# Kernel optimization log

Measured on AMD Instinct MI355X. Metric: run time of the kernel, lower is better.

## Reference

```python
import jax, jax.numpy as jnp
import numpy as np

N = 20000   # nodes
E = 320000  # edges (before self loops)
H = 4       # heads
HID = 64    # hidden per head
EMB = 32    # embedding dim
IN = 4      # input features
SLOPE = 0.2   # GATv2 leaky_relu negative slope
BN_EPS = 1e-5


def _gatv2(x, Wl, bl, Wr, br, att, bias, src, dst, heads, out_ch, concat, n_nodes):
    # PyG GATv2Conv (share_weights=False, add_self_loops handled by caller)
    xl = (x @ Wl.T + bl).reshape(n_nodes, heads, out_ch)  # source transform (x_j)
    xr = (x @ Wr.T + br).reshape(n_nodes, heads, out_ch)  # target transform (x_i)
    e = jax.nn.leaky_relu(xl[src] + xr[dst], SLOPE)       # [E, H, C]
    score = jnp.einsum('ehc,hc->eh', e, att)              # [E, H]
    smax = jax.ops.segment_max(score, dst, num_segments=n_nodes)
    expw = jnp.exp(score - smax[dst])
    denom = jax.ops.segment_sum(expw, dst, num_segments=n_nodes)
    alpha = expw / (denom[dst] + 1e-16)                   # segment softmax over dst
    out = jax.ops.segment_sum(xl[src] * alpha[:, :, None], dst, num_segments=n_nodes)
    out = out.reshape(n_nodes, heads * out_ch) if concat else out.mean(axis=1)
    return out + bias


def _bn(x, gamma, beta, mean, var):
    # BatchNorm1d, eval mode (running stats)
    return gamma * (x - mean) * jax.lax.rsqrt(var + BN_EPS) + beta


def setup_inputs() -> dict:
    key = jax.random.key(0)
    ks = iter(jax.random.split(key, 40))
    d = {}
    d['x'] = jax.random.normal(next(ks), (N, IN), dtype=jnp.float32)
    d['edge_index'] = jax.random.randint(next(ks), (2, E), 0, N, dtype=jnp.int32)

    def lin(k, o, i):
        return (jax.random.normal(k, (o, i), dtype=jnp.float32) * (1.0 / np.sqrt(i)))

    d['Wl1'] = lin(next(ks), H * HID, IN); d['bl1'] = jnp.zeros((H * HID,), jnp.float32)
    d['Wr1'] = lin(next(ks), H * HID, IN); d['br1'] = jnp.zeros((H * HID,), jnp.float32)
    d['att1'] = jax.random.normal(next(ks), (H, HID), dtype=jnp.float32) * 0.1
    d['bias1'] = jnp.zeros((H * HID,), jnp.float32)
    d['bn1_g'] = jnp.ones((H * HID,), jnp.float32)
    d['bn1_b'] = jnp.zeros((H * HID,), jnp.float32)
    d['bn1_m'] = jax.random.normal(next(ks), (H * HID,), dtype=jnp.float32) * 0.1
    d['bn1_v'] = jax.random.uniform(next(ks), (H * HID,), dtype=jnp.float32) + 0.5

    d['Wl2'] = lin(next(ks), H * HID, H * HID); d['bl2'] = jnp.zeros((H * HID,), jnp.float32)
    d['Wr2'] = lin(next(ks), H * HID, H * HID); d['br2'] = jnp.zeros((H * HID,), jnp.float32)
    d['att2'] = jax.random.normal(next(ks), (H, HID), dtype=jnp.float32) * 0.1
    d['bias2'] = jnp.zeros((H * HID,), jnp.float32)
    d['bn2_g'] = jnp.ones((H * HID,), jnp.float32)
    d['bn2_b'] = jnp.zeros((H * HID,), jnp.float32)
    d['bn2_m'] = jax.random.normal(next(ks), (H * HID,), dtype=jnp.float32) * 0.1
    d['bn2_v'] = jax.random.uniform(next(ks), (H * HID,), dtype=jnp.float32) + 0.5

    # layer 3: 256 -> 32, 1 head, mean (concat=False)
    d['Wl3'] = lin(next(ks), EMB, H * HID); d['bl3'] = jnp.zeros((EMB,), jnp.float32)
    d['Wr3'] = lin(next(ks), EMB, H * HID); d['br3'] = jnp.zeros((EMB,), jnp.float32)
    d['att3'] = jax.random.normal(next(ks), (1, EMB), dtype=jnp.float32) * 0.1
    d['bias3'] = jnp.zeros((EMB,), jnp.float32)
    return d


def reference(x, edge_index,
              Wl1, bl1, Wr1, br1, att1, bias1, bn1_g, bn1_b, bn1_m, bn1_v,
              Wl2, bl2, Wr2, br2, att2, bias2, bn2_g, bn2_b, bn2_m, bn2_v,
              Wl3, bl3, Wr3, br3, att3, bias3):
    # add self loops (PyG default add_self_loops=True)
    loops = jnp.arange(N, dtype=edge_index.dtype)
    src = jnp.concatenate([edge_index[0], loops])
    dst = jnp.concatenate([edge_index[1], loops])

    h = _gatv2(x, Wl1, bl1, Wr1, br1, att1, bias1, src, dst, H, HID, True, N)
    h = jax.nn.elu(_bn(h, bn1_g, bn1_b, bn1_m, bn1_v))  # dropout: eval mode -> identity
    h = _gatv2(h, Wl2, bl2, Wr2, br2, att2, bias2, src, dst, H, HID, True, N)
    h = jax.nn.elu(_bn(h, bn2_g, bn2_b, bn2_m, bn2_v))
    z = _gatv2(h, Wl3, bl3, Wr3, br3, att3, bias3, src, dst, 1, EMB, False, N)
    return z
```

## Files before the change

kernel.cpp:

```cpp
#include <hip/hip_runtime.h>
#include <math.h>

#define NN 20000
#define EE 320000
#define ETOT (EE + NN)
#define NSCAN ((NN + 1023) / 1024)

typedef unsigned short ushort_t;
typedef unsigned int uint_t;
typedef __attribute__((ext_vector_type(8))) short bf16x8;
typedef __attribute__((ext_vector_type(4))) float f32x4;

__device__ __forceinline__ ushort_t f2bf(float f) {
  union { float f; uint_t u; } v; v.f = f;
  uint_t r = v.u + 0x7FFF + ((v.u >> 16) & 1);
  return (ushort_t)(r >> 16);
}
__device__ __forceinline__ float bf2f(uint_t hi16) {
  union { uint_t u; float f; } v; v.u = hi16 << 16;
  return v.f;
}
__device__ __forceinline__ uint_t pack2(float a, float b) {
  return (uint_t)f2bf(a) | ((uint_t)f2bf(b) << 16);
}
__device__ __forceinline__ void unpack8(uint4 u, float* x) {
  x[0] = bf2f(u.x & 0xFFFF); x[1] = bf2f(u.x >> 16);
  x[2] = bf2f(u.y & 0xFFFF); x[3] = bf2f(u.y >> 16);
  x[4] = bf2f(u.z & 0xFFFF); x[5] = bf2f(u.z >> 16);
  x[6] = bf2f(u.w & 0xFFFF); x[7] = bf2f(u.w >> 16);
}

__global__ void deg_kernel(const int* __restrict__ ei, int* __restrict__ deg) {
  int e = blockIdx.x * 256 + threadIdx.x;
  if (e >= ETOT) return;
  int dst = (e < EE) ? ei[EE + e] : (e - EE);
  atomicAdd(&deg[dst], 1);
}

__global__ __launch_bounds__(1024) void scan1_kernel(const int* __restrict__ deg,
                                                     int* __restrict__ rowptr,
                                                     int* __restrict__ partials) {
  __shared__ int wsum[16];
  const int tid = threadIdx.x;
  const int lane = tid & 63, wid = tid >> 6;
  int i = blockIdx.x * 1024 + tid;
  int v = (i < NN) ? deg[i] : 0;
  int x = v;
  #pragma unroll
  for (int off = 1; off < 64; off <<= 1) {
    int y = __shfl_up(x, off, 64);
    if (lane >= off) x += y;
  }
  if (lane == 63) wsum[wid] = x;
  __syncthreads();
  if (tid < 64) {
    int w = (tid < 16) ? wsum[tid] : 0;
    #pragma unroll
    for (int off = 1; off < 16; off <<= 1) {
      int y = __shfl_up(w, off, 64);
      if (lane >= off) w += y;
    }
    if (tid < 16) wsum[tid] = w;
  }
  __syncthreads();
  int incl = x + (wid > 0 ? wsum[wid - 1] : 0);
  if (i < NN) rowptr[i] = incl - v;
  if (tid == 1023) partials[blockIdx.x] = incl;
}

__global__ void scan2_kernel(int* __restrict__ partials, int* __restrict__ rowptr) {
  int lane = threadIdx.x;
  int v = (lane < NSCAN) ? partials[lane] : 0;
  int x = v;
  #pragma unroll
  for (int off = 1; off < 64; off <<= 1) {
    int y = __shfl_up(x, off, 64);
    if (lane >= off) x += y;
  }
  if (lane < NSCAN) partials[lane] = x - v;
  if (lane == 63) rowptr[NN] = x;
}

__global__ __launch_bounds__(1024) void scan3_kernel(int* __restrict__ rowptr,
                                                     const int* __restrict__ partials,
                                                     int* __restrict__ cursor) {
  int i = blockIdx.x * 1024 + threadIdx.x;
  if (i < NN) {
    int r = rowptr[i] + partials[blockIdx.x];
    rowptr[i] = r;
    cursor[i] = r;
  }
}

__global__ void fill_kernel(const int* __restrict__ ei, int* __restrict__ cursor,
                            int* __restrict__ csr_src) {
  int e = blockIdx.x * 256 + threadIdx.x;
  if (e >= ETOT) return;
  int src, dst;
  if (e < EE) { src = ei[e]; dst = ei[EE + e]; } else { src = dst = e - EE; }
  int slot = atomicAdd(&cursor[dst], 1);
  csr_src[slot] = src;
}

__global__ void lin1_w2bf(const float* __restrict__ x,
                          const float* __restrict__ Wl, const float* __restrict__ bl,
                          const float* __restrict__ Wr, const float* __restrict__ br,
                          ushort_t* __restrict__ xlr,
                          const float* __restrict__ W0, const float* __restrict__ W1,
                          const float* __restrict__ W2, const float* __restrict__ W3,
                          ushort_t* __restrict__ Wb) {
  if (blockIdx.x >= NN) {
    int i = (blockIdx.x - NN) * 256 + threadIdx.x;
    if (i < 65536) Wb[i] = f2bf(W0[i]);
    else if (i < 131072) Wb[i] = f2bf(W1[i - 65536]);
    else if (i < 139264) Wb[i] = f2bf(W2[i - 131072]);
    else if (i < 147456) Wb[i] = f2bf(W3[i - 139264]);
    return;
  }
  int n = blockIdx.x, o = threadIdx.x;
  float4 xv = *reinterpret_cast<const float4*>(x + (size_t)n * 4);
  float4 wl = *reinterpret_cast<const float4*>(Wl + (size_t)o * 4);
  float4 wr = *reinterpret_cast<const float4*>(Wr + (size_t)o * 4);
  xlr[(size_t)n * 512 + o]       = f2bf(wl.x * xv.x + wl.y * xv.y + wl.z * xv.z + wl.w * xv.w + bl[o]);
  xlr[(size_t)n * 512 + 256 + o] = f2bf(wr.x * xv.x + wr.y * xv.y + wr.z * xv.z + wr.w * xv.w + br[o]);
}

template<int N, int NL, int WMW, int WNW>
__global__ __launch_bounds__(WMW * WNW * 64) void gemm_mfma(
    const ushort_t* __restrict__ X, const ushort_t* __restrict__ Wb,
    const float* __restrict__ bl, const float* __restrict__ br,
    ushort_t* __restrict__ Y, int M) {
  const int wave = threadIdx.x >> 6;
  const int lane = threadIdx.x & 63;
  const int wm = wave / WNW, wn = wave % WNW;
  const int r16 = lane & 15;
  const int koff = (lane >> 4) * 8;
  const int m0 = blockIdx.x * (WMW * 64) + wm * 64;
  const int nb = blockIdx.y * (WNW * 64) + wn * 64;

  const ushort_t* xp = X + (size_t)(m0 + r16) * 256 + koff;
  const ushort_t* wp = Wb + (size_t)(nb + r16) * 256 + koff;

  f32x4 acc[4][4] = {};
  bf16x8 A[4], B[4], An[4], Bn[4];
  #pragma unroll
  for (int i = 0; i < 4; ++i) {
    A[i] = *reinterpret_cast<const bf16x8*>(xp + i * 16 * 256);
    B[i] = *reinterpret_cast<const bf16x8*>(wp + i * 16 * 256);
  }
  #pragma unroll
  for (int t = 0; t < 8; ++t) {
    if (t < 7) {
      const int k0 = (t + 1) * 32;
      #pragma unroll
      for (int i = 0; i < 4; ++i) {
        An[i] = *reinterpret_cast<const bf16x8*>(xp + i * 16 * 256 + k0);
        Bn[i] = *reinterpret_cast<const bf16x8*>(wp + i * 16 * 256 + k0);
      }
    }
    #pragma unroll
    for (int j = 0; j < 4; ++j)
      #pragma unroll
      for (int i = 0; i < 4; ++i)
        acc[j][i] = __builtin_amdgcn_mfma_f32_16x16x32_bf16(B[j], A[i], acc[j][i], 0, 0, 0);
    #pragma unroll
    for (int i = 0; i < 4; ++i) { A[i] = An[i]; B[i] = Bn[i]; }
  }

  const int nlocal = (lane >> 4) * 2;
  #pragma unroll
  for (int j = 0; j < 4; ++j) {
    const int ncol0 = nb + j * 16 + (lane >> 4) * 4;
    const float4 bv = *reinterpret_cast<const float4*>(
        (ncol0 < NL) ? (bl + ncol0) : (br + (ncol0 - NL)));
    #pragma unroll
    for (int i = 0; i < 4; ++i) {
      int m = m0 + i * 16 + r16;
      if (m < M) {
        uint2 o;
        o.x = pack2(acc[j][i][0] + bv.x, acc[j][i][1] + bv.y);
        o.y = pack2(acc[j][i][2] + bv.z, acc[j][i][3] + bv.w);
        *reinterpret_cast<uint2*>(Y + (size_t)m * N + ncol0) = o;
      }
    }
  }
}

template<bool BN_ELU>
__global__ __launch_bounds__(256) void fused_agg4(
    const ushort_t* __restrict__ xlr,
    const int* __restrict__ rowptr, const int* __restrict__ csr_src,
    const float* __restrict__ att, const float* __restrict__ bias,
    const float* __restrict__ bn_g, const float* __restrict__ bn_b,
    const float* __restrict__ bn_m, const float* __restrict__ bn_v,
    ushort_t* __restrict__ out) {
  int n = blockIdx.x * 4 + (threadIdx.x >> 6);
  if (n >= NN) return;
  int lane = threadIdx.x & 63;
  int half = lane >> 5;
  int l32 = lane & 31;

  float xr[8], at[8];
  {
    uint4 xru = reinterpret_cast<const uint4*>(xlr + (size_t)n * 512 + 256)[l32];
    unpack8(xru, xr);
    float4 a0 = reinterpret_cast<const float4*>(att)[l32 * 2];
    float4 a1 = reinterpret_cast<const float4*>(att)[l32 * 2 + 1];
    at[0] = a0.x; at[1] = a0.y; at[2] = a0.z; at[3] = a0.w;
    at[4] = a1.x; at[5] = a1.y; at[6] = a1.z; at[7] = a1.w;
  }
  int beg = rowptr[n], end = rowptr[n + 1];

  float m = -3.4e38f, d = 0.f;
  float acc[8] = {0.f, 0.f, 0.f, 0.f, 0.f, 0.f, 0.f, 0.f};

  for (int s = beg + half; s < end; s += 2) {
    int src = csr_src[s];
    uint4 xu = reinterpret_cast<const uint4*>(xlr + (size_t)src * 512)[l32];
    float x[8];
    unpack8(xu, x);
    float sc = 0.f;
    #pragma unroll
    for (int c = 0; c < 8; ++c) {
      float e = x[c] + xr[c];
      e = fmaxf(e, 0.2f * e);
      sc = fmaf(at[c], e, sc);
    }
    #pragma unroll
    for (int off = 4; off; off >>= 1) sc += __shfl_xor(sc, off, 64);
    if (__any(sc > m + 8.f)) {
      float mn = fmaxf(m, sc);
      float scl = __expf(m - mn);
      float w = __expf(sc - mn);
      #pragma unroll
      for (int c = 0; c < 8; ++c) acc[c] = fmaf(w, x[c], acc[c] * scl);
      d = d * scl + w;
      m = mn;
    } else {
      float w = __expf(sc - m);
      #pragma unroll
      for (int c = 0; c < 8; ++c) acc[c] = fmaf(w, x[c], acc[c]);
      d += w;
    }
  }

  {
    float mo = __shfl_xor(m, 32, 64);
    float doo = __shfl_xor(d, 32, 64);
    float ao[8];
    #pragma unroll
    for (int c = 0; c < 8; ++c) ao[c] = __shfl_xor(acc[c], 32, 64);
    if (doo > 0.f) {
      if (d > 0.f) {
        float mn = fmaxf(m, mo);
        float se = __expf(m - mn), so = __expf(mo - mn);
        #pragma unroll
        for (int c = 0; c < 8; ++c) acc[c] = acc[c] * se + ao[c] * so;
        d = d * se + doo * so;
      } else {
        #pragma unroll
        for (int c = 0; c < 8; ++c) acc[c] = ao[c];
        d = doo;
      }
    }
  }

  if (half == 0) {
    float inv = 1.f / (d + 1e-16f);
    float4 b0 = reinterpret_cast<const float4*>(bias)[l32 * 2];
    float4 b1 = reinterpret_cast<const float4*>(bias)[l32 * 2 + 1];
    float v[8];
    v[0] = acc[0] * inv + b0.x; v[1] = acc[1] * inv + b0.y;
    v[2] = acc[2] * inv + b0.z; v[3] = acc[3] * inv + b0.w;
    v[4] = acc[4] * inv + b1.x; v[5] = acc[5] * inv + b1.y;
    v[6] = acc[6] * inv + b1.z; v[7] = acc[7] * inv + b1.w;
    if (BN_ELU) {
      float4 g0 = reinterpret_cast<const float4*>(bn_g)[l32 * 2];
      float4 g1 = reinterpret_cast<const float4*>(bn_g)[l32 * 2 + 1];
      float4 bb0 = reinterpret_cast<const float4*>(bn_b)[l32 * 2];
      float4 bb1 = reinterpret_cast<const float4*>(bn_b)[l32 * 2 + 1];
      float4 mu0 = reinterpret_cast<const float4*>(bn_m)[l32 * 2];
      float4 mu1 = reinterpret_cast<const float4*>(bn_m)[l32 * 2 + 1];
      float4 va0 = reinterpret_cast<const float4*>(bn_v)[l32 * 2];
      float4 va1 = reinterpret_cast<const float4*>(bn_v)[l32 * 2 + 1];
      float g[8] = {g0.x, g0.y, g0.z, g0.w, g1.x, g1.y, g1.z, g1.w};
      float bb[8] = {bb0.x, bb0.y, bb0.z, bb0.w, bb1.x, bb1.y, bb1.z, bb1.w};
      float mu[8] = {mu0.x, mu0.y, mu0.z, mu0.w, mu1.x, mu1.y, mu1.z, mu1.w};
      float va[8] = {va0.x, va0.y, va0.z, va0.w, va1.x, va1.y, va1.z, va1.w};
      #pragma unroll
      for (int c = 0; c < 8; ++c) {
        float sc = g[c] * rsqrtf(va[c] + 1e-5f);
        float t = sc * (v[c] - mu[c]) + bb[c];
        v[c] = (t > 0.f) ? t : expm1f(t);
      }
    }
    uint4 o;
    o.x = pack2(v[0], v[1]);
    o.y = pack2(v[2], v[3]);
    o.z = pack2(v[4], v[5]);
    o.w = pack2(v[6], v[7]);
    reinterpret_cast<uint4*>(out + (size_t)n * 256)[l32] = o;
  }
}

__global__ __launch_bounds__(256) void fused_agg3(
    const ushort_t* __restrict__ xlr,
    const int* __restrict__ rowptr, const int* __restrict__ csr_src,
    const float* __restrict__ att, const float* __restrict__ bias,
    float* __restrict__ out) {
  int n = blockIdx.x * 4 + (threadIdx.x >> 6);
  if (n >= NN) return;
  int lane = threadIdx.x & 63;
  int grp = lane >> 4;
  int cl = lane & 15;
  uint_t xru = reinterpret_cast<const uint_t*>(xlr + (size_t)n * 64 + 32)[cl];
  float xr0 = bf2f(xru & 0xFFFF), xr1 = bf2f(xru >> 16);
  float2 atv = reinterpret_cast<const float2*>(att)[cl];
  int beg = rowptr[n], end = rowptr[n + 1];
  float m = -3.4e38f, d = 0.f, a0 = 0.f, a1 = 0.f;
  for (int s = beg + grp; s < end; s += 4) {
    int src = csr_src[s];
    uint_t xu = reinterpret_cast<const uint_t*>(xlr + (size_t)src * 64)[cl];
    float x0 = bf2f(xu & 0xFFFF), x1 = bf2f(xu >> 16);
    float e0 = x0 + xr0; e0 = fmaxf(e0, 0.2f * e0);
    float e1 = x1 + xr1; e1 = fmaxf(e1, 0.2f * e1);
    float sc = fmaf(atv.x, e0, atv.y * e1);
    #pragma unroll
    for (int off = 8; off; off >>= 1) sc += __shfl_xor(sc, off, 64);
    if (__any(sc > m + 8.f)) {
      float mn = fmaxf(m, sc);
      float scale = __expf(m - mn);
      float w = __expf(sc - mn);
      a0 = fmaf(w, x0, a0 * scale);
      a1 = fmaf(w, x1, a1 * scale);
      d = d * scale + w;
      m = mn;
    } else {
      float w = __expf(sc - m);
      a0 = fmaf(w, x0, a0);
      a1 = fmaf(w, x1, a1);
      d += w;
    }
  }
  #pragma unroll
  for (int off = 16; off <= 32; off <<= 1) {
    float mo = __shfl_xor(m, off, 64);
    float doo = __shfl_xor(d, off, 64);
    float c0 = __shfl_xor(a0, off, 64);
    float c1 = __shfl_xor(a1, off, 64);
    if (doo > 0.f) {
      if (d > 0.f) {
        float mn = fmaxf(m, mo);
        float se = __expf(m - mn), so = __expf(mo - mn);
        a0 = a0 * se + c0 * so;
        a1 = a1 * se + c1 * so;
        d = d * se + doo * so;
        m = mn;
      } else {
        a0 = c0; a1 = c1; d = doo; m = mo;
      }
    }
  }
  if (grp == 0) {
    float inv = 1.f / (d + 1e-16f);
    float2 bsv = reinterpret_cast<const float2*>(bias)[cl];
    reinterpret_cast<float2*>(out + (size_t)n * 32)[cl] =
        make_float2(a0 * inv + bsv.x, a1 * inv + bsv.y);
  }
}

extern "C" void kernel_launch(void* const* d_in, const int* in_sizes, int n_in,
                              void* d_out, int out_size, void* d_ws, size_t ws_size,
                              hipStream_t stream) {
  (void)in_sizes; (void)n_in; (void)out_size; (void)ws_size;
  const float* x  = (const float*)d_in[0];
  const int*   ei = (const int*)d_in[1];
  const float *Wl1 = (const float*)d_in[2],  *bl1 = (const float*)d_in[3],
              *Wr1 = (const float*)d_in[4],  *br1 = (const float*)d_in[5],
              *att1 = (const float*)d_in[6], *bias1 = (const float*)d_in[7],
              *g1 = (const float*)d_in[8],   *be1 = (const float*)d_in[9],
              *m1 = (const float*)d_in[10],  *v1 = (const float*)d_in[11];
  const float *Wl2 = (const float*)d_in[12], *bl2 = (const float*)d_in[13],
              *Wr2 = (const float*)d_in[14], *br2 = (const float*)d_in[15],
              *att2 = (const float*)d_in[16], *bias2 = (const float*)d_in[17],
              *g2 = (const float*)d_in[18],  *be2 = (const float*)d_in[19],
              *m2 = (const float*)d_in[20],  *v2 = (const float*)d_in[21];
  const float *Wl3 = (const float*)d_in[22], *bl3 = (const float*)d_in[23],
              *Wr3 = (const float*)d_in[24], *br3 = (const float*)d_in[25],
              *att3 = (const float*)d_in[26], *bias3 = (const float*)d_in[27];
  float* out = (float*)d_out;

  char* p = (char*)d_ws;
  auto alloc = [&](size_t bytes) { char* r = p; p += (bytes + 255) & ~(size_t)255; return r; };
  int*      deg      = (int*)alloc((size_t)NN * 4);
  int*      rowptr   = (int*)alloc((size_t)(NN + 1) * 4);
  int*      cursor   = (int*)alloc((size_t)NN * 4);
  int*      partials = (int*)alloc((size_t)NSCAN * 4);
  int*      csr_src  = (int*)alloc((size_t)ETOT * 4);
  ushort_t* xlr      = (ushort_t*)alloc((size_t)NN * 512 * 2);
  ushort_t* hbuf     = (ushort_t*)alloc((size_t)NN * 256 * 2);
  ushort_t* Wb       = (ushort_t*)alloc((size_t)147456 * 2);
  (void)alloc(262144);

  hipMemsetAsync(deg, 0, (size_t)NN * 4, stream);
  deg_kernel<<<(ETOT + 255) / 256, 256, 0, stream>>>(ei, deg);
  scan1_kernel<<<NSCAN, 1024, 0, stream>>>(deg, rowptr, partials);
  scan2_kernel<<<1, 64, 0, stream>>>(partials, rowptr);
  scan3_kernel<<<NSCAN, 1024, 0, stream>>>(rowptr, partials, cursor);
  fill_kernel<<<(ETOT + 255) / 256, 256, 0, stream>>>(ei, cursor, csr_src);

  int nb = (NN + 3) / 4;

  lin1_w2bf<<<NN + 576, 256, 0, stream>>>(x, Wl1, bl1, Wr1, br1, xlr,
                                          Wl2, Wr2, Wl3, Wr3, Wb);
  fused_agg4<true><<<nb, 256, 0, stream>>>(xlr, rowptr, csr_src, att1, bias1,
                                           g1, be1, m1, v1, hbuf);

  {
    dim3 g((NN + 63) / 64, 2);
    gemm_mfma<512, 256, 1, 4><<<g, 256, 0, stream>>>(hbuf, Wb, bl2, br2, xlr, NN);
  }
  fused_agg4<true><<<nb, 256, 0, stream>>>(xlr, rowptr, csr_src, att2, bias2,
                                           g2, be2, m2, v2, hbuf);

  {
    dim3 g((NN + 255) / 256, 1);
    gemm_mfma<64, 32, 4, 1><<<g, 256, 0, stream>>>(hbuf, Wb + 131072, bl3, br3, xlr, NN);
  }
  fused_agg3<<<nb, 256, 0, stream>>>(xlr, rowptr, csr_src, att3, bias3, out);
}
```

Before: 206.4 us.

## Merge scan2 into scan3, fuse CSR fill with lin1, prefetch neighbor rows

The separate single-block scan2 kernel is removed. Each scan3 block now sums the preceding partials itself and the last block writes rowptr[NN]. The CSR fill kernel is merged into the lin1/weight-conversion launch as extra blocks, which removes two kernel launches and their serialization gaps. The aggregation loops in fused_agg4 and fused_agg3 software-prefetch the next neighbor's feature row one iteration ahead, to hide gather latency at the cost of extra registers and a redundant clamped load on the final iteration.

After: 185.0 us. 1.12x faster.

```diff
diff --git a/kernel.cpp b/kernel.cpp
--- a/kernel.cpp
+++ b/kernel.cpp
@@ -5,6 +5,7 @@
 #define EE 320000
 #define ETOT (EE + NN)
 #define NSCAN ((NN + 1023) / 1024)
+#define FILLB ((ETOT + 255) / 256)
 
 typedef unsigned short ushort_t;
 typedef unsigned int uint_t;
@@ -68,56 +69,55 @@
   if (tid == 1023) partials[blockIdx.x] = incl;
 }
 
-__global__ void scan2_kernel(int* __restrict__ partials, int* __restrict__ rowptr) {
-  int lane = threadIdx.x;
-  int v = (lane < NSCAN) ? partials[lane] : 0;
-  int x = v;
-  #pragma unroll
-  for (int off = 1; off < 64; off <<= 1) {
-    int y = __shfl_up(x, off, 64);
-    if (lane >= off) x += y;
-  }
-  if (lane < NSCAN) partials[lane] = x - v;
-  if (lane == 63) rowptr[NN] = x;
-}
-
 __global__ __launch_bounds__(1024) void scan3_kernel(int* __restrict__ rowptr,
                                                      const int* __restrict__ partials,
                                                      int* __restrict__ cursor) {
-  int i = blockIdx.x * 1024 + threadIdx.x;
+  __shared__ int off_s;
+  int tid = threadIdx.x;
+  if (tid < 64) {
+    int v = (tid < NSCAN && tid < (int)blockIdx.x) ? partials[tid] : 0;
+    #pragma unroll
+    for (int o = 32; o; o >>= 1) v += __shfl_xor(v, o, 64);
+    if (tid == 0) off_s = v;
+  }
+  __syncthreads();
+  int off = off_s;
+  int i = blockIdx.x * 1024 + tid;
   if (i < NN) {
-    int r = rowptr[i] + partials[blockIdx.x];
+    int r = rowptr[i] + off;
     rowptr[i] = r;
     cursor[i] = r;
   }
-}
-
-__global__ void fill_kernel(const int* __restrict__ ei, int* __restrict__ cursor,
-                            int* __restrict__ csr_src) {
-  int e = blockIdx.x * 256 + threadIdx.x;
-  if (e >= ETOT) return;
-  int src, dst;
-  if (e < EE) { src = ei[e]; dst = ei[EE + e]; } else { src = dst = e - EE; }
-  int slot = atomicAdd(&cursor[dst], 1);
-  csr_src[slot] = src;
-}
-
-__global__ void lin1_w2bf(const float* __restrict__ x,
-                          const float* __restrict__ Wl, const float* __restrict__ bl,
-                          const float* __restrict__ Wr, const float* __restrict__ br,
-                          ushort_t* __restrict__ xlr,
-                          const float* __restrict__ W0, const float* __restrict__ W1,
-                          const float* __restrict__ W2, const float* __restrict__ W3,
-                          ushort_t* __restrict__ Wb) {
-  if (blockIdx.x >= NN) {
-    int i = (blockIdx.x - NN) * 256 + threadIdx.x;
+  if (blockIdx.x == NSCAN - 1 && tid == 0) rowptr[NN] = off + partials[NSCAN - 1];
+}
+
+__global__ void fill_lin1_w2bf(const int* __restrict__ ei, int* __restrict__ cursor,
+                               int* __restrict__ csr_src,
+                               const float* __restrict__ x,
+                               const float* __restrict__ Wl, const float* __restrict__ bl,
+                               const float* __restrict__ Wr, const float* __restrict__ br,
+                               ushort_t* __restrict__ xlr,
+                               const float* __restrict__ W0, const float* __restrict__ W1,
+                               const float* __restrict__ W2, const float* __restrict__ W3,
+                               ushort_t* __restrict__ Wb) {
+  if (blockIdx.x < FILLB) {
+    int e = blockIdx.x * 256 + threadIdx.x;
+    if (e >= ETOT) return;
+    int src, dst;
+    if (e < EE) { src = ei[e]; dst = ei[EE + e]; } else { src = dst = e - EE; }
+    int slot = atomicAdd(&cursor[dst], 1);
+    csr_src[slot] = src;
+    return;
+  }
+  if (blockIdx.x >= FILLB + NN) {
+    int i = (blockIdx.x - FILLB - NN) * 256 + threadIdx.x;
     if (i < 65536) Wb[i] = f2bf(W0[i]);
     else if (i < 131072) Wb[i] = f2bf(W1[i - 65536]);
     else if (i < 139264) Wb[i] = f2bf(W2[i - 131072]);
     else if (i < 147456) Wb[i] = f2bf(W3[i - 139264]);
     return;
   }
-  int n = blockIdx.x, o = threadIdx.x;
+  int n = blockIdx.x - FILLB, o = threadIdx.x;
   float4 xv = *reinterpret_cast<const float4*>(x + (size_t)n * 4);
   float4 wl = *reinterpret_cast<const float4*>(Wl + (size_t)o * 4);
   float4 wr = *reinterpret_cast<const float4*>(Wr + (size_t)o * 4);
@@ -167,7 +167,6 @@
     for (int i = 0; i < 4; ++i) { A[i] = An[i]; B[i] = Bn[i]; }
   }
 
-  const int nlocal = (lane >> 4) * 2;
   #pragma unroll
   for (int j = 0; j < 4; ++j) {
     const int ncol0 = nb + j * 16 + (lane >> 4) * 4;
@@ -214,9 +213,15 @@
   float m = -3.4e38f, d = 0.f;
   float acc[8] = {0.f, 0.f, 0.f, 0.f, 0.f, 0.f, 0.f, 0.f};
 
-  for (int s = beg + half; s < end; s += 2) {
-    int src = csr_src[s];
-    uint4 xu = reinterpret_cast<const uint4*>(xlr + (size_t)src * 512)[l32];
+  int s = beg + half;
+  int sp = (s < end) ? s : (end - 1);
+  uint4 xu = reinterpret_cast<const uint4*>(xlr + (size_t)csr_src[sp] * 512)[l32];
+
+  for (; s < end; s += 2) {
+    int sn = s + 2;
+    int snp = (sn < end) ? sn : (end - 1);
+    uint4 xun = reinterpret_cast<const uint4*>(xlr + (size_t)csr_src[snp] * 512)[l32];
+
     float x[8];
     unpack8(xu, x);
     float sc = 0.f;
@@ -242,6 +247,7 @@
       for (int c = 0; c < 8; ++c) acc[c] = fmaf(w, x[c], acc[c]);
       d += w;
     }
+    xu = xun;
   }
 
   {
@@ -318,9 +324,16 @@
   float2 atv = reinterpret_cast<const float2*>(att)[cl];
   int beg = rowptr[n], end = rowptr[n + 1];
   float m = -3.4e38f, d = 0.f, a0 = 0.f, a1 = 0.f;
-  for (int s = beg + grp; s < end; s += 4) {
-    int src = csr_src[s];
-    uint_t xu = reinterpret_cast<const uint_t*>(xlr + (size_t)src * 64)[cl];
+
+  int s = beg + grp;
+  int sp = (s < end) ? s : (end - 1);
+  uint_t xu = reinterpret_cast<const uint_t*>(xlr + (size_t)csr_src[sp] * 64)[cl];
+
+  for (; s < end; s += 4) {
+    int sn = s + 4;
+    int snp = (sn < end) ? sn : (end - 1);
+    uint_t xun = reinterpret_cast<const uint_t*>(xlr + (size_t)csr_src[snp] * 64)[cl];
+
     float x0 = bf2f(xu & 0xFFFF), x1 = bf2f(xu >> 16);
     float e0 = x0 + xr0; e0 = fmaxf(e0, 0.2f * e0);
     float e1 = x1 + xr1; e1 = fmaxf(e1, 0.2f * e1);
@@ -341,6 +354,7 @@
       a1 = fmaf(w, x1, a1);
       d += w;
     }
+    xu = xun;
   }
   #pragma unroll
   for (int off = 16; off <= 32; off <<= 1) {
@@ -405,14 +419,12 @@
   hipMemsetAsync(deg, 0, (size_t)NN * 4, stream);
   deg_kernel<<<(ETOT + 255) / 256, 256, 0, stream>>>(ei, deg);
   scan1_kernel<<<NSCAN, 1024, 0, stream>>>(deg, rowptr, partials);
-  scan2_kernel<<<1, 64, 0, stream>>>(partials, rowptr);
   scan3_kernel<<<NSCAN, 1024, 0, stream>>>(rowptr, partials, cursor);
-  fill_kernel<<<(ETOT + 255) / 256, 256, 0, stream>>>(ei, cursor, csr_src);
 
   int nb = (NN + 3) / 4;
 
-  lin1_w2bf<<<NN + 576, 256, 0, stream>>>(x, Wl1, bl1, Wr1, br1, xlr,
-                                          Wl2, Wr2, Wl3, Wr3, Wb);
+  fill_lin1_w2bf<<<FILLB + NN + 576, 256, 0, stream>>>(
+      ei, cursor, csr_src, x, Wl1, bl1, Wr1, br1, xlr, Wl2, Wr2, Wl3, Wr3, Wb);
   fused_agg4<true><<<nb, 256, 0, stream>>>(xlr, rowptr, csr_src, att1, bias1,
                                            g1, be1, m1, v1, hbuf);
 
```
